# Kernel optimization log

Measured on AMD Instinct MI355X. Metric: run time of the kernel, lower is better.

The kernel has to match this reference:

```python
import jax, jax.numpy as jnp
import numpy as np

CHEB_K = 3


def cheb_gcn(x, node_emb, w_pool, b_pool):
    # x: [B, N, C], node_emb: [N, D], w_pool: [D, K, C, O], b_pool: [D, O]
    n = node_emb.shape[0]
    A = jax.nn.softmax(jax.nn.relu(node_emb @ node_emb.T), axis=1)  # [N, N]
    supports = [jnp.eye(n, dtype=x.dtype), A]
    for _ in range(2, CHEB_K):
        supports.append(2.0 * A @ supports[-1] - supports[-2])
    S = jnp.stack(supports, axis=0)  # [K, N, N]
    weights = jnp.einsum('nd,dkio->nkio', node_emb, w_pool)  # [N, K, C, O]
    bias = node_emb @ b_pool  # [N, O]
    x_g = jnp.einsum('knm,bmc->bnkc', S, x)  # [B, N, K, C]
    return jnp.einsum('bnki,nkio->bno', x_g, weights) + bias


def setup_inputs() -> dict:
    key = jax.random.key(0)
    ks = jax.random.split(key, 7)
    B, N, DIN, DOUT, E = 64, 1024, 64, 64, 16
    C = DIN + DOUT
    return {
        'x': jax.random.normal(ks[0], (B, N, DIN), jnp.float32),
        'state': jax.random.normal(ks[1], (B, N, DOUT), jnp.float32),
        'node_embeddings': jax.random.normal(ks[2], (N, E), jnp.float32),
        'W_gate': jax.random.normal(ks[3], (E, CHEB_K, C, 2 * DOUT), jnp.float32) * 0.1,
        'b_gate': jax.random.normal(ks[4], (E, 2 * DOUT), jnp.float32) * 0.1,
        'W_update': jax.random.normal(ks[5], (E, CHEB_K, C, DOUT), jnp.float32) * 0.1,
        'b_update': jax.random.normal(ks[6], (E, DOUT), jnp.float32) * 0.1,
    }


def reference(x, state, node_embeddings, W_gate, b_gate, W_update, b_update):
    hidden = state.shape[-1]
    inp = jnp.concatenate([x, state], axis=-1)  # [B, N, DIN+DOUT]
    z_r = jax.nn.sigmoid(cheb_gcn(inp, node_embeddings, W_gate, b_gate))
    z, r = z_r[..., :hidden], z_r[..., hidden:]
    cand = jnp.concatenate([x, r * state], axis=-1)
    h_hat = jnp.tanh(cheb_gcn(cand, node_embeddings, W_update, b_update))
    return z * state + (1.0 - z) * h_hat
```

## Files before the change

kernel.cpp:

```cpp
#include <hip/hip_runtime.h>
#include <hip/hip_bf16.h>
#include <math.h>

#define B_ 64
#define N_ 1024
#define E_ 16

typedef unsigned short ushort_t;
typedef __attribute__((ext_vector_type(8))) short bf16x8;
typedef __attribute__((ext_vector_type(4))) float f32x4;

__device__ __forceinline__ float sigmoidf_(float x) {
  return 1.0f / (1.0f + __expf(-x));
}
__device__ __forceinline__ ushort_t f2bf(float f) {
  unsigned int u = __float_as_uint(f);
  u = (u + 0x7fffu + ((u >> 16) & 1u)) >> 16;
  return (ushort_t)u;
}
__device__ __forceinline__ float bf2f(ushort_t h) { return __uint_as_float((unsigned)h << 16); }
__device__ __forceinline__ void gload16(const void* g, void* l) {
  __builtin_amdgcn_global_load_lds(
      (const __attribute__((address_space(1))) unsigned int*)g,
      (__attribute__((address_space(3))) unsigned int*)l, 16, 0, 0);
}

__global__ __launch_bounds__(256) void compute_A_kernel(const float* __restrict__ emb,
                                                        ushort_t* __restrict__ Ah,
                                                        ushort_t* __restrict__ Al) {
  __shared__ float embn[E_];
  __shared__ float red[256];
  const int n = blockIdx.x;
  const int t = threadIdx.x;
  if (t < E_) embn[t] = emb[n * E_ + t];
  __syncthreads();
  float s[4];
#pragma unroll
  for (int j = 0; j < 4; ++j) {
    const int m = j * 256 + t;
    const float* em = emb + m * E_;
    float acc = 0.f;
#pragma unroll
    for (int d = 0; d < E_; ++d) acc = fmaf(embn[d], em[d], acc);
    s[j] = fmaxf(acc, 0.f);
  }
  float mx = fmaxf(fmaxf(s[0], s[1]), fmaxf(s[2], s[3]));
  red[t] = mx;
  __syncthreads();
  for (int off = 128; off > 0; off >>= 1) {
    if (t < off) red[t] = fmaxf(red[t], red[t + off]);
    __syncthreads();
  }
  mx = red[0];
  __syncthreads();
  float e[4], lsum = 0.f;
#pragma unroll
  for (int j = 0; j < 4; ++j) { e[j] = __expf(s[j] - mx); lsum += e[j]; }
  red[t] = lsum;
  __syncthreads();
  for (int off = 128; off > 0; off >>= 1) {
    if (t < off) red[t] += red[t + off];
    __syncthreads();
  }
  const float inv = 1.0f / red[0];
#pragma unroll
  for (int j = 0; j < 4; ++j) {
    const float v = e[j] * inv;
    ushort_t h = f2bf(v);
    Ah[n * N_ + j * 256 + t] = h;
    Al[n * N_ + j * 256 + t] = f2bf(v - bf2f(h));
  }
}

__global__ __launch_bounds__(256) void build_T0t_kernel(const float* __restrict__ xA,
                                                        const float* __restrict__ xB,
                                                        ushort_t* __restrict__ Th,
                                                        ushort_t* __restrict__ Tl) {
  __shared__ float tile[128][129];
  const int t = threadIdx.x;
  const int b = blockIdx.y;
  const int n0 = blockIdx.x << 7;
  const int c4 = (t & 31) << 2, nl = t >> 5;
#pragma unroll
  for (int p = 0; p < 16; ++p) {
    const int n = nl + (p << 3);
    const float4 v = (c4 < 64)
        ? *(const float4*)&xA[((size_t)b << 16) + ((size_t)(n0 + n) << 6) + c4]
        : *(const float4*)&xB[((size_t)b << 16) + ((size_t)(n0 + n) << 6) + c4 - 64];
    tile[c4 + 0][n] = v.x; tile[c4 + 1][n] = v.y;
    tile[c4 + 2][n] = v.z; tile[c4 + 3][n] = v.w;
  }
  __syncthreads();
  const int c = t >> 1, nc = (t & 1) << 6;
  const size_t obase = ((size_t)(b << 7) + c) * 1024 + n0 + nc;
#pragma unroll
  for (int u = 0; u < 64; u += 4) {
    ushort4 h, l;
    float v0 = tile[c][nc + u + 0], v1 = tile[c][nc + u + 1];
    float v2 = tile[c][nc + u + 2], v3 = tile[c][nc + u + 3];
    h.x = f2bf(v0); l.x = f2bf(v0 - bf2f(h.x));
    h.y = f2bf(v1); l.y = f2bf(v1 - bf2f(h.y));
    h.z = f2bf(v2); l.z = f2bf(v2 - bf2f(h.z));
    h.w = f2bf(v3); l.w = f2bf(v3 - bf2f(h.w));
    *(ushort4*)&Th[obase + u] = h;
    *(ushort4*)&Tl[obase + u] = l;
  }
}

template <int PHASE>
__global__ __launch_bounds__(256, 2) void mfma_gemm_kernel(
    const ushort_t* __restrict__ Ah, const ushort_t* __restrict__ Al,
    const ushort_t* __restrict__ Bh, const ushort_t* __restrict__ Bl,
    ushort_t* __restrict__ Yth, ushort_t* __restrict__ Ytl,
    ushort_t* __restrict__ XpH, ushort_t* __restrict__ XpL) {
  __shared__ ushort_t smem[4 * 128 * 64];
  ushort_t* Ah_s = smem;
  ushort_t* Al_s = smem + 8192;
  ushort_t* Bh_s = smem + 16384;
  ushort_t* Bl_s = smem + 24576;
  const int t = threadIdx.x;
  const int wave = t >> 6, lane = t & 63;
  const int n0 = blockIdx.y << 7;
  const int bcol = blockIdx.x;
  const int j0 = bcol << 7;
  const int wr = wave >> 1, wc = wave & 1;
  const int fr = lane & 15, fk = lane >> 4;

  f32x4 acc[4][4];
#pragma unroll
  for (int i = 0; i < 4; ++i)
#pragma unroll
    for (int j = 0; j < 4; ++j) acc[i][j] = (f32x4){0.f, 0.f, 0.f, 0.f};

  const int rsub = lane >> 3;
  const int cp = lane & 7;
  const int selem = (((cp << 4) ^ (rsub << 4)) >> 1);

  for (int k0 = 0; k0 < 1024; k0 += 64) {
    __syncthreads();
#pragma unroll
    for (int i = 0; i < 4; ++i) {
      const int q = (wave << 2) + i;
      const int row = (q << 3) + rsub;
      const int lo = (q << 9) + lane * 8;
      const size_t ga = (size_t)(n0 + row) * 1024 + k0 + selem;
      const size_t gb = (size_t)(j0 + row) * 1024 + k0 + selem;
      gload16(Ah + ga, Ah_s + lo);
      gload16(Al + ga, Al_s + lo);
      gload16(Bh + gb, Bh_s + lo);
      gload16(Bl + gb, Bl_s + lo);
    }
    __syncthreads();
#pragma unroll
    for (int ks = 0; ks < 2; ++ks) {
      bf16x8 ah[4], al[4], bh[4], bl[4];
#pragma unroll
      for (int mi = 0; mi < 4; ++mi) {
        const int r = (wr << 6) + (mi << 4) + fr;
        const int kb = ((ks << 6) + (fk << 4)) ^ ((r & 7) << 4);
        ah[mi] = *(const bf16x8*)((const char*)Ah_s + r * 128 + kb);
        al[mi] = *(const bf16x8*)((const char*)Al_s + r * 128 + kb);
      }
#pragma unroll
      for (int nj = 0; nj < 4; ++nj) {
        const int r = (wc << 6) + (nj << 4) + fr;
        const int kb = ((ks << 6) + (fk << 4)) ^ ((r & 7) << 4);
        bh[nj] = *(const bf16x8*)((const char*)Bh_s + r * 128 + kb);
        bl[nj] = *(const bf16x8*)((const char*)Bl_s + r * 128 + kb);
      }
#pragma unroll
      for (int mi = 0; mi < 4; ++mi)
#pragma unroll
        for (int nj = 0; nj < 4; ++nj) {
          acc[mi][nj] = __builtin_amdgcn_mfma_f32_16x16x32_bf16(ah[mi], bh[nj], acc[mi][nj], 0, 0, 0);
          acc[mi][nj] = __builtin_amdgcn_mfma_f32_16x16x32_bf16(ah[mi], bl[nj], acc[mi][nj], 0, 0, 0);
          acc[mi][nj] = __builtin_amdgcn_mfma_f32_16x16x32_bf16(al[mi], bh[nj], acc[mi][nj], 0, 0, 0);
        }
    }
  }

  __syncthreads();
  ushort_t* hiT = smem;
  ushort_t* loT = smem + 16384;
#pragma unroll
  for (int mi = 0; mi < 4; ++mi) {
    const int nl = (wr << 6) + (mi << 4) + (fk << 2);
#pragma unroll
    for (int nj = 0; nj < 4; ++nj) {
      const int jl = (wc << 6) + (nj << 4) + fr;
      const f32x4 vv = acc[mi][nj];
      ushort_t h[4], l[4];
#pragma unroll
      for (int r = 0; r < 4; ++r) {
        const float v = (PHASE == 1) ? vv[r] : 2.0f * vv[r];
        h[r] = f2bf(v);
        l[r] = f2bf(v - bf2f(h[r]));
      }
      if (PHASE == 1) {
        *(ushort4*)&Yth[(size_t)(j0 + jl) * 1024 + n0 + nl] = make_ushort4(h[0], h[1], h[2], h[3]);
        *(ushort4*)&Ytl[(size_t)(j0 + jl) * 1024 + n0 + nl] = make_ushort4(l[0], l[1], l[2], l[3]);
      }
#pragma unroll
      for (int r = 0; r < 4; ++r) {
        hiT[(nl + r) * 128 + jl] = h[r];
        loT[(nl + r) * 128 + jl] = l[r];
      }
    }
  }
  __syncthreads();
#pragma unroll
  for (int rr = 0; rr < 8; ++rr) {
    const int id = rr * 256 + t;
    const int nl = id >> 4, ch = id & 15;
    const size_t dstE = ((size_t)(n0 + nl) * 64 + bcol) * 256 + ch * 8;
    *(uint4*)&XpH[dstE] = *(const uint4*)((const char*)hiT + nl * 256 + ch * 16);
    *(uint4*)&XpL[dstE] = *(const uint4*)((const char*)loT + nl * 256 + ch * 16);
  }
}

template <int OW>
__global__ __launch_bounds__(256) void wpt_kernel(const float* __restrict__ Wp,
                                                  float* __restrict__ WpT) {
  const int idx = blockIdx.x * 256 + threadIdx.x;
  const int ki = idx % 384;
  const int k = ki >> 7, i = ki & 127;
  const int o = idx / 384;
  float v[16];
#pragma unroll
  for (int d = 0; d < 16; ++d) v[d] = Wp[((size_t)d * 384 + ki) * OW + o];
  if (k == 0) {
#pragma unroll
    for (int d = 0; d < 16; ++d) v[d] -= Wp[((size_t)d * 384 + 256 + i) * OW + o];
  }
  float* dst = WpT + (size_t)idx * 16;
#pragma unroll
  for (int q = 0; q < 4; ++q) *(float4*)&dst[q * 4] = *(const float4*)&v[q * 4];
}

__global__ __launch_bounds__(384) void wcombine5_kernel(const float* __restrict__ emb,
                                                        const float* __restrict__ WpT,
                                                        ushort_t* __restrict__ WtH,
                                                        ushort_t* __restrict__ WtL) {
  __shared__ float embs[256 * 16];
  __shared__ ushort_t sH[8 * 384];
  __shared__ ushort_t sL[8 * 384];
  const int t = threadIdx.x;
  const int o = blockIdx.y;
  const int n0 = blockIdx.x << 8;
  for (int i = t; i < 1024; i += 384)
    *(float4*)&embs[i * 4] = *(const float4*)&emb[(size_t)n0 * 16 + i * 4];
  float wreg[16];
  {
    const float* src = WpT + (size_t)o * 6144 + t * 16;
#pragma unroll
    for (int q = 0; q < 4; ++q) *(float4*)&wreg[q * 4] = *(const float4*)&src[q * 4];
  }
  __syncthreads();
  for (int g = 0; g < 32; ++g) {
#pragma unroll
    for (int nl = 0; nl < 8; ++nl) {
      const float* e = &embs[(g * 8 + nl) * 16];
      float a = 0.f;
#pragma unroll
      for (int d = 0; d < 16; ++d) a = fmaf(e[d], wreg[d], a);
      const ushort_t h = f2bf(a);
      sH[nl * 384 + t] = h;
      sL[nl * 384 + t] = f2bf(a - bf2f(h));
    }
    __syncthreads();
    const size_t ob = ((size_t)o * 1024 + n0 + g * 8) * 384 + t * 8;
    *(uint4*)&WtH[ob] = *(const uint4*)&sH[t * 8];
    *(uint4*)&WtL[ob] = *(const uint4*)&sL[t * 8];
    __syncthreads();
  }
}

template <int MODE>
__global__ __launch_bounds__(256, 2) void pernode_mfma_kernel(
    const float* __restrict__ xA, const float* __restrict__ xB,
    const ushort_t* __restrict__ XpH, const ushort_t* __restrict__ XpL,
    const ushort_t* __restrict__ WtH, const ushort_t* __restrict__ WtL,
    const float* __restrict__ emb, const float* __restrict__ bsrc, int bstride,
    const float* __restrict__ state, const float* __restrict__ zb,
    float* __restrict__ dst) {
  __shared__ ushort_t xh_s[64 * 128];
  __shared__ ushort_t xl_s[64 * 128];
  __shared__ ushort_t wh_s[64 * 128];
  __shared__ ushort_t wl_s[64 * 128];
  __shared__ float embn[E_];
  __shared__ float bias[64];
  const int n = blockIdx.x;
  const int t = threadIdx.x;
  if (t < E_) embn[t] = emb[n * E_ + t];
  __syncthreads();
  if (t < 64) {
    float a = 0.f;
#pragma unroll
    for (int d = 0; d < E_; ++d) a = fmaf(embn[d], bsrc[d * bstride + t], a);
    bias[t] = a;
  }
  const int wave = t >> 6, lane = t & 63;
  const int fr = lane & 15, fq = lane >> 4;
  f32x4 acc[4];
#pragma unroll
  for (int i = 0; i < 4; ++i) acc[i] = (f32x4){0.f, 0.f, 0.f, 0.f};

#pragma unroll
  for (int s = 0; s < 3; ++s) {
    __syncthreads();
    if (s == 0) {
      const int b = t >> 2, q = t & 3;
      const float* srcp = (q < 2)
          ? xA + ((size_t)b << 16) + ((size_t)n << 6) + (q << 5)
          : xB + ((size_t)b << 16) + ((size_t)n << 6) + ((q - 2) << 5);
      float v[32];
#pragma unroll
      for (int j = 0; j < 8; ++j) *(float4*)&v[j * 4] = *(const float4*)&srcp[j * 4];
      const int swz = (b & 7) << 4;
#pragma unroll
      for (int jc = 0; jc < 4; ++jc) {
        unsigned int hh[4], ll[4];
#pragma unroll
        for (int e = 0; e < 4; ++e) {
          const float a0 = v[jc * 8 + 2 * e], a1 = v[jc * 8 + 2 * e + 1];
          const ushort_t h0 = f2bf(a0), h1 = f2bf(a1);
          const ushort_t l0 = f2bf(a0 - bf2f(h0)), l1 = f2bf(a1 - bf2f(h1));
          hh[e] = (unsigned)h0 | ((unsigned)h1 << 16);
          ll[e] = (unsigned)l0 | ((unsigned)l1 << 16);
        }
        const int dstb = b * 256 + (((q << 6) + (jc << 4)) ^ swz);
        *(uint4*)((char*)xh_s + dstb) = make_uint4(hh[0], hh[1], hh[2], hh[3]);
        *(uint4*)((char*)xl_s + dstb) = make_uint4(ll[0], ll[1], ll[2], ll[3]);
      }
    } else {
#pragma unroll
      for (int r = 0; r < 4; ++r) {
        const int id = r * 256 + t;
        const int row = id >> 4, ch = id & 15;
        const int selem = (((ch << 4) ^ ((row & 7) << 4)) >> 1);
        const size_t so = ((size_t)n * 64 + row) * 256 + (s - 1) * 128 + selem;
        gload16(XpH + so, xh_s + id * 8);
        gload16(XpL + so, xl_s + id * 8);
      }
    }
#pragma unroll
    for (int r = 0; r < 4; ++r) {
      const int id = r * 256 + t;
      const int row = id >> 4, ch = id & 15;
      const int selem = (((ch << 4) ^ ((row & 7) << 4)) >> 1);
      const size_t so = ((size_t)row * 1024 + n) * 384 + s * 128 + selem;
      gload16(WtH + so, wh_s + id * 8);
      gload16(WtL + so, wl_s + id * 8);
    }
    __syncthreads();
#pragma unroll
    for (int ks = 0; ks < 4; ++ks) {
      bf16x8 ah[4], al[4];
#pragma unroll
      for (int mi = 0; mi < 4; ++mi) {
        const int r = (mi << 4) + fr;
        const int kb = ((ks << 6) + (fq << 4)) ^ ((r & 7) << 4);
        ah[mi] = *(const bf16x8*)((const char*)xh_s + r * 256 + kb);
        al[mi] = *(const bf16x8*)((const char*)xl_s + r * 256 + kb);
      }
      const int rw = (wave << 4) + fr;
      const int kbw = ((ks << 6) + (fq << 4)) ^ ((rw & 7) << 4);
      const bf16x8 wh = *(const bf16x8*)((const char*)wh_s + rw * 256 + kbw);
      const bf16x8 wl = *(const bf16x8*)((const char*)wl_s + rw * 256 + kbw);
#pragma unroll
      for (int mi = 0; mi < 4; ++mi) {
        acc[mi] = __builtin_amdgcn_mfma_f32_16x16x32_bf16(ah[mi], wh, acc[mi], 0, 0, 0);
        acc[mi] = __builtin_amdgcn_mfma_f32_16x16x32_bf16(al[mi], wh, acc[mi], 0, 0, 0);
        acc[mi] = __builtin_amdgcn_mfma_f32_16x16x32_bf16(ah[mi], wl, acc[mi], 0, 0, 0);
      }
    }
  }

  const int o = (wave << 4) + fr;
  const float bia = bias[o];
#pragma unroll
  for (int mi = 0; mi < 4; ++mi) {
    const int b0 = (mi << 4) + (fq << 2);
    const f32x4 vv = acc[mi];
#pragma unroll
    for (int r = 0; r < 4; ++r) {
      const int b = b0 + r;
      const size_t base = ((size_t)b << 16) + ((size_t)n << 6);
      const float a = vv[r] + bia;
      if (MODE == 0) {
        dst[base + o] = sigmoidf_(a);
      } else if (MODE == 1) {
        dst[base + o] = sigmoidf_(a) * state[base + o];
      } else {
        const float z = zb[base + o], st = state[base + o];
        dst[base + o] = z * st + (1.f - z) * tanhf(a);
      }
    }
  }
}

extern "C" void kernel_launch(void* const* d_in, const int* in_sizes, int n_in,
                              void* d_out, int out_size, void* d_ws, size_t ws_size,
                              hipStream_t stream) {
  const float* x     = (const float*)d_in[0];
  const float* state = (const float*)d_in[1];
  const float* emb   = (const float*)d_in[2];
  const float* Wg    = (const float*)d_in[3];
  const float* bg    = (const float*)d_in[4];
  const float* Wu    = (const float*)d_in[5];
  const float* bu    = (const float*)d_in[6];
  float* out = (float*)d_out;

  char* w = (char*)d_ws;
  ushort_t* Ah   = (ushort_t*)(w);
  ushort_t* Al   = (ushort_t*)(w + ((size_t)2 << 20));
  ushort_t* T0th = (ushort_t*)(w + ((size_t)4 << 20));
  ushort_t* T0tl = (ushort_t*)(w + ((size_t)20 << 20));
  ushort_t* Y1th = (ushort_t*)(w + ((size_t)36 << 20));
  ushort_t* Y1tl = (ushort_t*)(w + ((size_t)52 << 20));
  ushort_t* XpH  = (ushort_t*)(w + ((size_t)68 << 20));
  ushort_t* XpL  = (ushort_t*)(w + ((size_t)100 << 20));
  ushort_t* WtH  = (ushort_t*)(w + ((size_t)132 << 20));
  ushort_t* WtL  = (ushort_t*)(w + ((size_t)180 << 20));
  float*    rs   = (float*)(w + ((size_t)228 << 20));
  float*    WpTg = (float*)(w + ((size_t)244 << 20));
  float*    WpTu = (float*)(w + ((size_t)247 << 20));
  float* zb = out;

  const dim3 gg(64, 8);
  const dim3 gt(8, 64);
  const dim3 gc(4, 64);

  compute_A_kernel<<<N_, 256, 0, stream>>>(emb, Ah, Al);
  wpt_kernel<128><<<192, 256, 0, stream>>>(Wg, WpTg);
  wpt_kernel<64><<<96, 256, 0, stream>>>(Wu, WpTu);

  build_T0t_kernel<<<gt, 256, 0, stream>>>(x, state, T0th, T0tl);
  mfma_gemm_kernel<1><<<gg, 256, 0, stream>>>(Ah, Al, T0th, T0tl, Y1th, Y1tl, XpH, XpL);
  mfma_gemm_kernel<0><<<gg, 256, 0, stream>>>(Ah, Al, Y1th, Y1tl, nullptr, nullptr,
                                              XpH + 128, XpL + 128);
  wcombine5_kernel<<<gc, 384, 0, stream>>>(emb, WpTg, WtH, WtL);
  pernode_mfma_kernel<0><<<N_, 256, 0, stream>>>(x, state, XpH, XpL, WtH, WtL, emb, bg, 128,
                                                 state, nullptr, zb);
  wcombine5_kernel<<<gc, 384, 0, stream>>>(emb, WpTg + (size_t)64 * 6144, WtH, WtL);
  pernode_mfma_kernel<1><<<N_, 256, 0, stream>>>(x, state, XpH, XpL, WtH, WtL, emb, bg + 64, 128,
                                                 state, nullptr, rs);

  wcombine5_kernel<<<gc, 384, 0, stream>>>(emb, WpTu, WtH, WtL);
  build_T0t_kernel<<<gt, 256, 0, stream>>>(x, rs, T0th, T0tl);
  mfma_gemm_kernel<1><<<gg, 256, 0, stream>>>(Ah, Al, T0th, T0tl, Y1th, Y1tl, XpH, XpL);
  mfma_gemm_kernel<0><<<gg, 256, 0, stream>>>(Ah, Al, Y1th, Y1tl, nullptr, nullptr,
                                              XpH + 128, XpL + 128);
  pernode_mfma_kernel<2><<<N_, 256, 0, stream>>>(x, rs, XpH, XpL, WtH, WtL, emb, bu, 64,
                                                 state, zb, out);
}
```

Before: 524.4 us.

## Skip recomputing graph propagation of x channels in the update GCN

The update-phase candidate input concatenates x with r*state, and the x part's graph propagation (A·x, A·A·x) is identical to what the gate phase already computed. The change transposes only the 64 r*state channels, runs the two propagation GEMMs on half the columns, and scatters their results into the upper half of each per-node channel slot in the existing Xp buffers. This relies on the x-channel entries left over from the gate phase staying valid in XpH/XpL, which ties correctness to buffer reuse order.

```diff
diff --git a/kernel.cpp b/kernel.cpp
--- a/kernel.cpp
+++ b/kernel.cpp
@@ -107,7 +107,39 @@
   }
 }
 
-template <int PHASE>
+__global__ __launch_bounds__(256) void build_T0s_kernel(const float* __restrict__ rs,
+                                                        ushort_t* __restrict__ Th,
+                                                        ushort_t* __restrict__ Tl) {
+  __shared__ float tile[64][129];
+  const int t = threadIdx.x;
+  const int b = blockIdx.y;
+  const int n0 = blockIdx.x << 7;
+  const int c4 = (t & 15) << 2, nl = t >> 4;
+#pragma unroll
+  for (int p = 0; p < 8; ++p) {
+    const int n = nl + (p << 4);
+    const float4 v = *(const float4*)&rs[((size_t)b << 16) + ((size_t)(n0 + n) << 6) + c4];
+    tile[c4 + 0][n] = v.x; tile[c4 + 1][n] = v.y;
+    tile[c4 + 2][n] = v.z; tile[c4 + 3][n] = v.w;
+  }
+  __syncthreads();
+  const int c = t >> 2, nc = (t & 3) << 5;
+  const size_t obase = ((size_t)(b << 6) + c) * 1024 + n0 + nc;
+#pragma unroll
+  for (int u = 0; u < 32; u += 4) {
+    ushort4 h, l;
+    float v0 = tile[c][nc + u + 0], v1 = tile[c][nc + u + 1];
+    float v2 = tile[c][nc + u + 2], v3 = tile[c][nc + u + 3];
+    h.x = f2bf(v0); l.x = f2bf(v0 - bf2f(h.x));
+    h.y = f2bf(v1); l.y = f2bf(v1 - bf2f(h.y));
+    h.z = f2bf(v2); l.z = f2bf(v2 - bf2f(h.z));
+    h.w = f2bf(v3); l.w = f2bf(v3 - bf2f(h.w));
+    *(ushort4*)&Th[obase + u] = h;
+    *(ushort4*)&Tl[obase + u] = l;
+  }
+}
+
+template <int PHASE, int SPAN>
 __global__ __launch_bounds__(256, 2) void mfma_gemm_kernel(
     const ushort_t* __restrict__ Ah, const ushort_t* __restrict__ Al,
     const ushort_t* __restrict__ Bh, const ushort_t* __restrict__ Bl,
@@ -212,7 +244,13 @@
   for (int rr = 0; rr < 8; ++rr) {
     const int id = rr * 256 + t;
     const int nl = id >> 4, ch = id & 15;
-    const size_t dstE = ((size_t)(n0 + nl) * 64 + bcol) * 256 + ch * 8;
+    size_t dstE;
+    if (SPAN == 128) {
+      dstE = ((size_t)(n0 + nl) * 64 + bcol) * 256 + ch * 8;
+    } else {
+      const int bb = bcol * 2 + (ch >> 3);
+      dstE = ((size_t)(n0 + nl) * 64 + bb) * 256 + 64 + (ch & 7) * 8;
+    }
     *(uint4*)&XpH[dstE] = *(const uint4*)((const char*)hiT + nl * 256 + ch * 16);
     *(uint4*)&XpL[dstE] = *(const uint4*)((const char*)loT + nl * 256 + ch * 16);
   }
@@ -428,6 +466,7 @@
   float* zb = out;
 
   const dim3 gg(64, 8);
+  const dim3 gu(32, 8);
   const dim3 gt(8, 64);
   const dim3 gc(4, 64);
 
@@ -436,9 +475,9 @@
   wpt_kernel<64><<<96, 256, 0, stream>>>(Wu, WpTu);
 
   build_T0t_kernel<<<gt, 256, 0, stream>>>(x, state, T0th, T0tl);
-  mfma_gemm_kernel<1><<<gg, 256, 0, stream>>>(Ah, Al, T0th, T0tl, Y1th, Y1tl, XpH, XpL);
-  mfma_gemm_kernel<0><<<gg, 256, 0, stream>>>(Ah, Al, Y1th, Y1tl, nullptr, nullptr,
-                                              XpH + 128, XpL + 128);
+  mfma_gemm_kernel<1, 128><<<gg, 256, 0, stream>>>(Ah, Al, T0th, T0tl, Y1th, Y1tl, XpH, XpL);
+  mfma_gemm_kernel<0, 128><<<gg, 256, 0, stream>>>(Ah, Al, Y1th, Y1tl, nullptr, nullptr,
+                                                   XpH + 128, XpL + 128);
   wcombine5_kernel<<<gc, 384, 0, stream>>>(emb, WpTg, WtH, WtL);
   pernode_mfma_kernel<0><<<N_, 256, 0, stream>>>(x, state, XpH, XpL, WtH, WtL, emb, bg, 128,
                                                  state, nullptr, zb);
@@ -447,10 +486,10 @@
                                                  state, nullptr, rs);
 
   wcombine5_kernel<<<gc, 384, 0, stream>>>(emb, WpTu, WtH, WtL);
-  build_T0t_kernel<<<gt, 256, 0, stream>>>(x, rs, T0th, T0tl);
-  mfma_gemm_kernel<1><<<gg, 256, 0, stream>>>(Ah, Al, T0th, T0tl, Y1th, Y1tl, XpH, XpL);
-  mfma_gemm_kernel<0><<<gg, 256, 0, stream>>>(Ah, Al, Y1th, Y1tl, nullptr, nullptr,
-                                              XpH + 128, XpL + 128);
+  build_T0s_kernel<<<gt, 256, 0, stream>>>(rs, T0th, T0tl);
+  mfma_gemm_kernel<1, 64><<<gu, 256, 0, stream>>>(Ah, Al, T0th, T0tl, Y1th, Y1tl, XpH, XpL);
+  mfma_gemm_kernel<0, 64><<<gu, 256, 0, stream>>>(Ah, Al, Y1th, Y1tl, nullptr, nullptr,
+                                                  XpH + 128, XpL + 128);
   pernode_mfma_kernel<2><<<N_, 256, 0, stream>>>(x, rs, XpH, XpL, WtH, WtL, emb, bu, 64,
                                                  state, zb, out);
 }
```

New measurement: 489.7 us. -6.6%, faster.
